# Optimization experiments

Hardware: AMD Instinct MI355X
Metric: run time of the kernel (lower is better)

Reference implementation:

```python
import jax, jax.numpy as jnp
import numpy as np
from jax import lax

DIM = 256
HEADS = 8
DIM_HEAD = 32
INNER = HEADS * DIM_HEAD  # 256
SCALE = DIM_HEAD ** -0.5
EPS = 1e-5
DN = ('NCHW', 'OIHW', 'NCHW')


def chan_layer_norm(x, g):
    # LayerNorm over channel dim (axis=1), biased variance
    mean = jnp.mean(x, axis=1, keepdims=True)
    var = jnp.mean((x - mean) ** 2, axis=1, keepdims=True)
    return (x - mean) / jnp.sqrt(var + EPS) * g


def conv1x1(x, w):
    return lax.conv_general_dilated(x, w, (1, 1), 'VALID', dimension_numbers=DN)


def dwconv3x3(x, w):
    # depthwise 3x3, padding=1, groups=channels; w: [C,1,3,3]
    return lax.conv_general_dilated(x, w, (1, 1), 'SAME', dimension_numbers=DN,
                                    feature_group_count=x.shape[1])


def setup_inputs() -> dict:
    key = jax.random.key(0)
    ks = jax.random.split(key, 9)
    B, X, Y = 16, 64, 64
    fmap = jax.random.normal(ks[0], (B, DIM, X, Y), dtype=jnp.float32)
    w = lambda k, shape: (jax.random.normal(k, shape, dtype=jnp.float32) * 0.02)
    return {
        'fmap': fmap,
        'g_norm': jnp.ones((1, DIM, 1, 1), dtype=jnp.float32),
        'wq1': w(ks[1], (INNER, DIM, 1, 1)),
        'wq_dw': w(ks[2], (INNER, 1, 3, 3)),
        'wk1': w(ks[3], (INNER, DIM, 1, 1)),
        'wk_dw': w(ks[4], (INNER, 1, 3, 3)),
        'wv1': w(ks[5], (INNER, DIM, 1, 1)),
        'wv_dw': w(ks[6], (INNER, 1, 3, 3)),
        'wo': w(ks[7], (DIM, INNER, 1, 1)),
        'g_out': jnp.ones((1, DIM, 1, 1), dtype=jnp.float32),
    }


def reference(fmap, g_norm, wq1, wq_dw, wk1, wk_dw, wv1, wv_dw, wo, g_out):
    b, _, X, Y = fmap.shape
    n = X * Y
    x = chan_layer_norm(fmap, g_norm)
    # QKV: 1x1 conv -> depthwise 3x3 conv (dropout is identity in eval)
    q = dwconv3x3(conv1x1(x, wq1), wq_dw)
    k = dwconv3x3(conv1x1(x, wk1), wk_dw)
    v = dwconv3x3(conv1x1(x, wv1), wv_dw)
    # b (h c) x y -> b h n c
    def split(t):
        return t.reshape(b, HEADS, DIM_HEAD, n).transpose(0, 1, 3, 2)
    q, k, v = split(q), split(k), split(v)
    q = jax.nn.softmax(q, axis=-1) * SCALE   # softmax over feature dim
    k = jax.nn.softmax(k, axis=-2)           # softmax over sequence dim
    ctx = jnp.einsum('bhnd,bhne->bhde', k, v)    # [b,h,d,d]
    out = jnp.einsum('bhnd,bhde->bhne', q, ctx)  # [b,h,n,d]
    # b h n d -> b (h d) x y
    out = out.transpose(0, 1, 3, 2).reshape(b, INNER, X, Y)
    out = jax.nn.silu(out)
    out = conv1x1(out, wo)
    return chan_layer_norm(out, g_out)
```

## Files before the change

kernel.cpp:

```cpp
#include <hip/hip_runtime.h>


typedef unsigned short u16;
typedef __bf16 bf16x8 __attribute__((ext_vector_type(8)));
typedef float f32x4 __attribute__((ext_vector_type(4)));
typedef float f32x16 __attribute__((ext_vector_type(16)));

#define DEV static __device__ __forceinline__

DEV float b2f(u16 u) { return __uint_as_float(((unsigned int)u) << 16); }
DEV u16 f2bf(float f) {
  unsigned int u = __float_as_uint(f);
  return (u16)((u + 0x7fffu + ((u >> 16) & 1u)) >> 16);
}
DEV void gl2lds16(const void* g, void* l) {
  __builtin_amdgcn_global_load_lds((__attribute__((address_space(1))) void*)g,
                                   (__attribute__((address_space(3))) void*)l, 16, 0, 0);
}

__global__ __launch_bounds__(256) void prep_kernel(const float* __restrict__ wk,
                                                   const float* __restrict__ wv,
                                                   const float* __restrict__ wq,
                                                   const float* __restrict__ wo,
                                                   u16* __restrict__ wb) {
  const int i = blockIdx.x * 256 + threadIdx.x;
  const int yb = blockIdx.y;
  if (yb == 0)      wb[(i >> 8) * 512 + (i & 255)] = f2bf(wk[i]);
  else if (yb == 1) wb[(i >> 8) * 512 + 256 + (i & 255)] = f2bf(wv[i]);
  else if (yb == 2) wb[131072 + i] = f2bf(wq[i]);
  else              wb[196608 + i] = f2bf(wo[i]);
}

__global__ __launch_bounds__(256) void ln_tin_kernel(const float* __restrict__ f,
                                                     const float* __restrict__ g,
                                                     u16* __restrict__ xT) {
  __shared__ u16 tile[64 * 268];
  __shared__ float red[2 * 256];
  __shared__ float mu_s[64], inv_s[64];
  const int t = threadIdx.x;
  const int p0 = blockIdx.x * 64;
  const int b = blockIdx.y;
  const long fb = (long)b * 256 * 4096;
  const int p = t & 63, cg = t >> 6;
  float s1 = 0.f, s2 = 0.f;
  for (int pass = 0; pass < 64; ++pass) {
    int c = pass * 4 + cg;
    float v = f[fb + (long)c * 4096 + p0 + p];
    s1 += v; s2 += v * v;
    tile[p * 268 + c] = f2bf(v);
  }
  red[cg * 64 + p] = s1;
  red[256 + cg * 64 + p] = s2;
  __syncthreads();
  if (t < 64) {
    float a1 = red[t] + red[64 + t] + red[128 + t] + red[192 + t];
    float a2 = red[256 + t] + red[320 + t] + red[384 + t] + red[448 + t];
    float mu = a1 * (1.f / 256.f);
    float var = a2 * (1.f / 256.f) - mu * mu;
    mu_s[t] = mu;
    inv_s[t] = 1.0f / sqrtf(var + 1e-5f);
  }
  __syncthreads();
  {
    const int ch8 = (t & 31) * 8, wp = t >> 5;
    float ga[8];
#pragma unroll
    for (int e = 0; e < 8; ++e) ga[e] = g[ch8 + e];
#pragma unroll
    for (int pass = 0; pass < 8; ++pass) {
      const int px = pass * 8 + wp;
      uint2 lo = *(const uint2*)&tile[px * 268 + ch8];
      uint2 hi = *(const uint2*)&tile[px * 268 + ch8 + 4];
      const u16* sl = (const u16*)&lo;
      const u16* sh = (const u16*)&hi;
      const float mu = mu_s[px], inv = inv_s[px];
      uint4 o;
      u16* os = (u16*)&o;
#pragma unroll
      for (int e = 0; e < 4; ++e) os[e] = f2bf((b2f(sl[e]) - mu) * inv * ga[e]);
#pragma unroll
      for (int e = 0; e < 4; ++e) os[4 + e] = f2bf((b2f(sh[e]) - mu) * inv * ga[4 + e]);
      *(uint4*)&xT[((long)b * 4096 + p0 + px) * 256 + ch8] = o;
    }
  }
}

__global__ __launch_bounds__(256) void gemm_bt_kernel(
    const u16* __restrict__ A, const u16* __restrict__ B0, const u16* __restrict__ B1,
    u16* __restrict__ Cg, int ldc, long sA, long sC) {
  __shared__ u16 As[128 * 32];
  __shared__ u16 Bs[128 * 32];
  const int t = threadIdx.x;
  const int wave = t >> 6, lane = t & 63, quad = lane >> 4, l16 = lane & 15;
  const int wr = wave >> 1, wc = wave & 1;
  const int m0 = blockIdx.x * 128;
  const int jt = blockIdx.y;
  const int b = blockIdx.z;
  const u16* Ab = A + (long)b * sA + (long)m0 * 256;
  const u16* Bt = (jt < 2 ? B0 : B1) + (jt & 1) * 128 * 256;
  u16* Cb = Cg + (long)b * sC + (long)m0 * ldc + jt * 128;

  const int srow = lane >> 2;
  const int scol = (lane & 3) * 8;
  f32x4 acc[4][4];
#pragma unroll
  for (int i = 0; i < 4; ++i)
#pragma unroll
    for (int j = 0; j < 4; ++j) acc[i][j] = (f32x4){0.f, 0.f, 0.f, 0.f};

  const int aoff = (wr * 64 + l16) * 32 + quad * 8;
  const int boff = (wc * 64 + l16) * 32 + quad * 8;

  for (int ks = 0; ks < 8; ++ks) {
    const int k0 = ks * 32;
    __syncthreads();
    for (int i = wave; i < 8; i += 4) {
      gl2lds16(Ab + (i * 16 + srow) * 256 + k0 + scol, &As[i * 512 + lane * 8]);
      gl2lds16(Bt + (i * 16 + srow) * 256 + k0 + scol, &Bs[i * 512 + lane * 8]);
    }
    __syncthreads();
    bf16x8 af[4], bfr[4];
#pragma unroll
    for (int mt = 0; mt < 4; ++mt) af[mt] = *(const bf16x8*)&As[aoff + mt * 512];
#pragma unroll
    for (int nt = 0; nt < 4; ++nt) bfr[nt] = *(const bf16x8*)&Bs[boff + nt * 512];
#pragma unroll
    for (int mt = 0; mt < 4; ++mt)
#pragma unroll
      for (int nt = 0; nt < 4; ++nt)
        acc[mt][nt] = __builtin_amdgcn_mfma_f32_16x16x32_bf16(af[mt], bfr[nt], acc[mt][nt], 0, 0, 0);
  }
#pragma unroll
  for (int mt = 0; mt < 4; ++mt) {
    const int mbase = wr * 64 + mt * 16 + quad * 4;
#pragma unroll
    for (int nt = 0; nt < 4; ++nt) {
      const int n = wc * 64 + nt * 16 + l16;
#pragma unroll
      for (int r = 0; r < 4; ++r)
        Cb[(long)(mbase + r) * ldc + n] = f2bf(acc[mt][nt][r]);
    }
  }
}

__global__ __launch_bounds__(256) void dwq_kernel(const u16* __restrict__ qT,
                                                  const float* __restrict__ wdw,
                                                  u16* __restrict__ qp) {
  __shared__ u16 tile[6 * 66 * 40];
  const int t = threadIdx.x;
  const int strip = blockIdx.x, h = blockIdx.y, b = blockIdx.z;
  const int x0 = strip * 4;
  const int wave = t >> 6, lane = t & 63;
  const int ysel = lane & 15, cg = lane >> 4;
  const int y = wave * 16 + ysel;
  const int ty = t >> 2, tc = t & 3;

  if (t < 48) {
    const int slot = t >> 3, brd = (t >> 2) & 1, c4 = t & 3;
    *(uint4*)&tile[slot * 2640 + (brd ? 65 * 40 : 0) + c4 * 8] = (uint4){0, 0, 0, 0};
  }
  const u16* qrow = qT + (long)b * 4096 * 256 + h * 32 + tc * 8;
#pragma unroll
  for (int s = 0; s < 6; ++s) {
    const int xx = x0 - 1 + s;
    uint4 v = (uint4){0, 0, 0, 0};
    if ((unsigned)xx < 64u) v = *(const uint4*)(qrow + (long)(xx * 64 + ty) * 256);
    *(uint4*)&tile[s * 2640 + (ty + 1) * 40 + tc * 8] = v;
  }
  float w[72];
#pragma unroll
  for (int q = 0; q < 8; ++q)
#pragma unroll
    for (int i = 0; i < 9; ++i) w[q * 9 + i] = wdw[(h * 32 + cg * 8 + q) * 9 + i];
  __syncthreads();

  u16* ob = qp + ((long)b * 4096 + y) * 256 + h * 32 + cg * 8;
#pragma unroll
  for (int it = 0; it < 4; ++it) {
    const int x = x0 + it;
    float acc[8] = {0.f, 0.f, 0.f, 0.f, 0.f, 0.f, 0.f, 0.f};
#pragma unroll
    for (int r = 0; r < 3; ++r) {
#pragma unroll
      for (int dy = 0; dy < 3; ++dy) {
        uint4 pk = *(const uint4*)&tile[(it + r) * 2640 + (y + dy) * 40 + cg * 8];
        const u16* s = (const u16*)&pk;
#pragma unroll
        for (int q = 0; q < 8; ++q)
          acc[q] = fmaf(w[q * 9 + r * 3 + dy], b2f(s[q]), acc[q]);
      }
    }
    float e[8];
    float s = 0.f;
#pragma unroll
    for (int q = 0; q < 8; ++q) { e[q] = __expf(acc[q]); s += e[q]; }
    s += __shfl_xor(s, 16);
    s += __shfl_xor(s, 32);
    const float inv = 0.17677669529663687f / s;
    uint4 o;
    u16* os = (u16*)&o;
#pragma unroll
    for (int q = 0; q < 8; ++q) os[q] = f2bf(e[q] * inv);
    *(uint4*)(ob + (long)x * 16384) = o;
  }
}

__global__ __launch_bounds__(1024, 4) void ctx_kernel(const u16* __restrict__ kvT,
                                                      const float* __restrict__ wkdw,
                                                      const float* __restrict__ wvdw,
                                                      float* __restrict__ par0,
                                                      float* __restrict__ par1) {
  __shared__ float redb[8 * 1088];
  __shared__ float redk[16 * 32];
  const int t = threadIdx.x;
  const int strip = blockIdx.x, h = blockIdx.y, b = blockIdx.z;
  const int wave = t >> 6, lane = t & 63;
  const int g = wave >> 2, wq = wave & 3;
  const int x0 = strip * 32 + g * 8;
  const int c = lane & 31, half = lane >> 5;
  const int ystart = wq * 16 + half * 8;
  float wk[9], wv[9];
#pragma unroll
  for (int i = 0; i < 9; ++i) {
    wk[i] = wkdw[(h * 32 + c) * 9 + i];
    wv[i] = wvdw[(h * 32 + c) * 9 + i];
  }
  const u16* kb = kvT + (long)b * 4096 * 512 + 2 * (h * 32 + c);

  float fk[3][10], fv[3][10];
  unsigned pk[10];
#pragma unroll
  for (int r = 0; r < 2; ++r) {
    const int x = x0 - 1 + r;
#pragma unroll
    for (int m = 0; m < 10; ++m) {
      const int yy = ystart - 1 + m;
      float a = 0.f, bb = 0.f;
      if (((unsigned)x < 64u) & ((unsigned)yy < 64u)) {
        const unsigned u = *(const unsigned*)(kb + (long)(x * 64 + yy) * 512);
        a = b2f((u16)(u & 0xffffu));
        bb = b2f((u16)(u >> 16));
      }
      fk[r][m] = a; fv[r][m] = bb;
    }
  }
#pragma unroll
  for (int m = 0; m < 10; ++m) {
    const int yy = ystart - 1 + m;
    unsigned u = 0;
    if (((unsigned)(x0 + 1) < 64u) & ((unsigned)yy < 64u))
      u = *(const unsigned*)(kb + (long)((x0 + 1) * 64 + yy) * 512);
    pk[m] = u;
  }
#pragma unroll
  for (int m = 0; m < 10; ++m) {
    fk[2][m] = __uint_as_float(pk[m] << 16);
    fv[2][m] = __uint_as_float(pk[m] & 0xffff0000u);
  }
  f32x16 acc;
#pragma unroll
  for (int r = 0; r < 16; ++r) acc[r] = 0.f;
  float ks = 0.f;

  for (int it = 0; it < 8; ++it) {
    const int xn = x0 + it + 2;
#pragma unroll
    for (int m = 0; m < 10; ++m) {
      const int yy = ystart - 1 + m;
      unsigned u = 0;
      if (((unsigned)xn < 64u) & ((unsigned)yy < 64u))
        u = *(const unsigned*)(kb + (long)(xn * 64 + yy) * 512);
      pk[m] = u;
    }
    union { bf16x8 v; u16 s[8]; } af, bf_;
#pragma unroll
    for (int j = 0; j < 8; ++j) {
      float a = 0.f, bb = 0.f;
#pragma unroll
      for (int r = 0; r < 3; ++r)
#pragma unroll
        for (int dy = 0; dy < 3; ++dy) {
          a = fmaf(wk[r * 3 + dy], fk[r][j + dy], a);
          bb = fmaf(wv[r * 3 + dy], fv[r][j + dy], bb);
        }
      const u16 eb = f2bf(__expf(a));
      ks += b2f(eb);
      af.s[j] = eb;
      bf_.s[j] = f2bf(bb);
    }
    acc = __builtin_amdgcn_mfma_f32_32x32x16_bf16(af.v, bf_.v, acc, 0, 0, 0);
#pragma unroll
    for (int m = 0; m < 10; ++m) {
      fk[0][m] = fk[1][m]; fv[0][m] = fv[1][m];
      fk[1][m] = fk[2][m]; fv[1][m] = fv[2][m];
      fk[2][m] = __uint_as_float(pk[m] << 16);
      fv[2][m] = __uint_as_float(pk[m] & 0xffff0000u);
    }
  }
  ks += __shfl_xor(ks, 32);
  if (half == 0) redk[wave * 32 + c] = ks;
  if (wave >= 8) {
#pragma unroll
    for (int r = 0; r < 16; ++r) redb[(wave - 8) * 1088 + lane * 17 + r] = acc[r];
  }
  __syncthreads();
  if (wave < 8) {
#pragma unroll
    for (int r = 0; r < 16; ++r) acc[r] += redb[wave * 1088 + lane * 17 + r];
  }
  __syncthreads();
  if (wave >= 4 && wave < 8) {
#pragma unroll
    for (int r = 0; r < 16; ++r) redb[(wave - 4) * 1088 + lane * 17 + r] = acc[r];
  }
  __syncthreads();
  if (wave < 4) {
#pragma unroll
    for (int r = 0; r < 16; ++r) acc[r] += redb[wave * 1088 + lane * 17 + r];
  }
  __syncthreads();
  if (wave >= 1 && wave < 4) {
#pragma unroll
    for (int r = 0; r < 16; ++r) redb[(wave - 1) * 1088 + lane * 17 + r] = acc[r];
  }
  __syncthreads();
  if (wave == 0) {
    float* par = (strip ? par1 : par0) + (long)(b * 8 + h) * 1056;
#pragma unroll
    for (int r = 0; r < 16; ++r) {
      float sum = acc[r] + redb[lane * 17 + r] + redb[1088 + lane * 17 + r] +
                  redb[2176 + lane * 17 + r];
      const int d = (r & 3) + 8 * (r >> 2) + 4 * half;
      par[d * 32 + c] = sum;
    }
    if (t < 32) {
      float s = 0.f;
#pragma unroll
      for (int w = 0; w < 16; ++w) s += redk[w * 32 + t];
      par[1024 + t] = s;
    }
  }
}

__global__ __launch_bounds__(256) void attn_o_ln_kernel(const u16* __restrict__ qp,
                                                        const float* __restrict__ par0,
                                                        const float* __restrict__ par1,
                                                        const u16* __restrict__ wo_bf,
                                                        const float* __restrict__ gout,
                                                        float* __restrict__ out) {
  __shared__ char smem[77312];
  u16* cnhi = (u16*)smem;
  u16* cnlo = (u16*)(smem + 20480);
  u16* ytile = (u16*)smem;
  u16* stile = (u16*)(smem + 40960);
  float* redS = (float*)(smem + 74752);
  float* redQ = (float*)(smem + 75776);
  float* mu_s = (float*)(smem + 76800);
  float* inv_s = (float*)(smem + 77056);
  const int t = threadIdx.x;
  const int p0 = blockIdx.x * 64;
  const int b = blockIdx.z;
  const int wave = t >> 6, lane = t & 63, quad = lane >> 4, l16 = lane & 15;

  for (int j = 0; j < 32; ++j) {
    const int lidx = j * 256 + t;
    const int e = lidx & 31, d = (lidx >> 5) & 31, h = lidx >> 10;
    const long base = (long)(b * 8 + h) * 1056;
    const float ks = par0[base + 1024 + d] + par1[base + 1024 + d];
    const float c = (par0[base + d * 32 + e] + par1[base + d * 32 + e]) / ks;
    const u16 hi = f2bf(c);
    cnhi[h * 1280 + e * 40 + d] = hi;
    cnlo[h * 1280 + e * 40 + d] = f2bf(c - b2f(hi));
  }
  __syncthreads();

  {
    const u16* qb = qp + ((long)b * 4096 + p0 + wave * 16) * 256;
    const int srow = wave * 16 + quad * 4;
#pragma unroll
    for (int h = 0; h < 8; ++h) {
      const int cb = h * 1280 + quad * 8;
      const bf16x8 bhi0 = *(const bf16x8*)&cnhi[cb + l16 * 40];
      const bf16x8 bhi1 = *(const bf16x8*)&cnhi[cb + (16 + l16) * 40];
      const bf16x8 blo0 = *(const bf16x8*)&cnlo[cb + l16 * 40];
      const bf16x8 blo1 = *(const bf16x8*)&cnlo[cb + (16 + l16) * 40];
      const bf16x8 af = *(const bf16x8*)&qb[l16 * 256 + h * 32 + quad * 8];
      f32x4 a0 = (f32x4){0.f, 0.f, 0.f, 0.f};
      f32x4 a1 = (f32x4){0.f, 0.f, 0.f, 0.f};
      a0 = __builtin_amdgcn_mfma_f32_16x16x32_bf16(af, blo0, a0, 0, 0, 0);
      a0 = __builtin_amdgcn_mfma_f32_16x16x32_bf16(af, bhi0, a0, 0, 0, 0);
      a1 = __builtin_amdgcn_mfma_f32_16x16x32_bf16(af, blo1, a1, 0, 0, 0);
      a1 = __builtin_amdgcn_mfma_f32_16x16x32_bf16(af, bhi1, a1, 0, 0, 0);
#pragma unroll
      for (int r = 0; r < 4; ++r) {
        const int row = srow + r;
        const float v0 = a0[r], v1 = a1[r];
        stile[row * 264 + h * 32 + l16] = f2bf(v0 / (1.f + __expf(-v0)));
        stile[row * 264 + h * 32 + 16 + l16] = f2bf(v1 / (1.f + __expf(-v1)));
      }
    }
  }
  __syncthreads();

  {
    const int n0 = wave * 64;
    f32x4 acc[4][4];
#pragma unroll
    for (int i = 0; i < 4; ++i)
#pragma unroll
      for (int j = 0; j < 4; ++j) acc[i][j] = (f32x4){0.f, 0.f, 0.f, 0.f};
#pragma unroll
    for (int ks = 0; ks < 8; ++ks) {
      const int k0 = ks * 32;
      bf16x8 af[4], bfr[4];
#pragma unroll
      for (int mt = 0; mt < 4; ++mt)
        af[mt] = *(const bf16x8*)&stile[(mt * 16 + l16) * 264 + k0 + quad * 8];
#pragma unroll
      for (int nt = 0; nt < 4; ++nt)
        bfr[nt] = *(const bf16x8*)&wo_bf[(n0 + nt * 16 + l16) * 256 + k0 + quad * 8];
#pragma unroll
      for (int mt = 0; mt < 4; ++mt)
#pragma unroll
        for (int nt = 0; nt < 4; ++nt)
          acc[mt][nt] = __builtin_amdgcn_mfma_f32_16x16x32_bf16(af[mt], bfr[nt], acc[mt][nt], 0, 0, 0);
    }
#pragma unroll
    for (int mt = 0; mt < 4; ++mt) {
      const int rb = mt * 16 + quad * 4;
      float ls1[4] = {0.f, 0.f, 0.f, 0.f};
      float ls2[4] = {0.f, 0.f, 0.f, 0.f};
#pragma unroll
      for (int nt = 0; nt < 4; ++nt) {
        const int col = n0 + nt * 16 + l16;
#pragma unroll
        for (int r = 0; r < 4; ++r) {
          const u16 bv = f2bf(acc[mt][nt][r]);
          ytile[(rb + r) * 258 + col] = bv;
          const float yb = b2f(bv);
          ls1[r] += yb;
          ls2[r] += yb * yb;
        }
      }
#pragma unroll
      for (int r = 0; r < 4; ++r) {
        float a = ls1[r], q2 = ls2[r];
        a += __shfl_xor(a, 1); q2 += __shfl_xor(q2, 1);
        a += __shfl_xor(a, 2); q2 += __shfl_xor(q2, 2);
        a += __shfl_xor(a, 4); q2 += __shfl_xor(q2, 4);
        a += __shfl_xor(a, 8); q2 += __shfl_xor(q2, 8);
        if (l16 == 0) {
          redS[(rb + r) * 4 + wave] = a;
          redQ[(rb + r) * 4 + wave] = q2;
        }
      }
    }
  }
  __syncthreads();

  if (t < 64) {
    float s1 = redS[t * 4] + redS[t * 4 + 1] + redS[t * 4 + 2] + redS[t * 4 + 3];
    float s2 = redQ[t * 4] + redQ[t * 4 + 1] + redQ[t * 4 + 2] + redQ[t * 4 + 3];
    float mu = s1 * (1.f / 256.f);
    float var = s2 * (1.f / 256.f) - mu * mu;
    mu_s[t] = mu;
    inv_s[t] = 1.0f / sqrtf(var + 1e-5f);
  }
  __syncthreads();
  {
    const int lpx = t & 63, cw = t >> 6;
    const long ob = (long)b * 256 * 4096;
    const float mu = mu_s[lpx], inv = inv_s[lpx];
#pragma unroll
    for (int pass = 0; pass < 16; ++pass) {
      const int c4 = pass * 16 + cw * 4;
      const unsigned w0 = *(const unsigned*)&ytile[lpx * 258 + c4];
      const unsigned w1 = *(const unsigned*)&ytile[lpx * 258 + c4 + 2];
      out[ob + (long)(c4 + 0) * 4096 + p0 + lpx] = (b2f((u16)(w0 & 0xffffu)) - mu) * inv * gout[c4 + 0];
      out[ob + (long)(c4 + 1) * 4096 + p0 + lpx] = (b2f((u16)(w0 >> 16)) - mu) * inv * gout[c4 + 1];
      out[ob + (long)(c4 + 2) * 4096 + p0 + lpx] = (b2f((u16)(w1 & 0xffffu)) - mu) * inv * gout[c4 + 2];
      out[ob + (long)(c4 + 3) * 4096 + p0 + lpx] = (b2f((u16)(w1 >> 16)) - mu) * inv * gout[c4 + 3];
    }
  }
}

extern "C" void kernel_launch(void* const* d_in, const int* in_sizes, int n_in,
                              void* d_out, int out_size, void* d_ws, size_t ws_size,
                              hipStream_t stream) {
  (void)in_sizes; (void)n_in; (void)out_size; (void)ws_size;
  const float* fmap = (const float*)d_in[0];
  const float* gnorm = (const float*)d_in[1];
  const float* wq1 = (const float*)d_in[2];
  const float* wqdw = (const float*)d_in[3];
  const float* wk1 = (const float*)d_in[4];
  const float* wkdw = (const float*)d_in[5];
  const float* wv1 = (const float*)d_in[6];
  const float* wvdw = (const float*)d_in[7];
  const float* wo = (const float*)d_in[8];
  const float* gout = (const float*)d_in[9];
  float* out = (float*)d_out;
  char* ws = (char*)d_ws;

  float* par0 = (float*)(ws);
  u16* wb = (u16*)(ws + 540672);
  float* par1 = (float*)(ws + 1064960);
  u16* wkv_bf = wb;
  u16* wq_bf = wb + 131072;
  u16* wo_bf = wb + 196608;
  u16* xT = (u16*)(ws + 2097152);
  u16* kvT = (u16*)(ws + 35651584);
  u16* qT = kvT;
  u16* qp = (u16*)(ws + 69206016);

  prep_kernel<<<dim3(256, 4), 256, 0, stream>>>(wk1, wv1, wq1, wo, wb);
  ln_tin_kernel<<<dim3(64, 16), 256, 0, stream>>>(fmap, gnorm, xT);
  gemm_bt_kernel<<<dim3(32, 4, 16), 256, 0, stream>>>(xT, wkv_bf, wkv_bf + 65536, kvT, 512,
                                                      4096L * 256, 4096L * 512);
  ctx_kernel<<<dim3(2, 8, 16), 1024, 0, stream>>>(kvT, wkdw, wvdw, par0, par1);
  gemm_bt_kernel<<<dim3(32, 2, 16), 256, 0, stream>>>(xT, wq_bf, wq_bf, qT, 256,
                                                      4096L * 256, 4096L * 256);
  dwq_kernel<<<dim3(16, 8, 16), 256, 0, stream>>>(qT, wqdw, qp);
  attn_o_ln_kernel<<<dim3(64, 1, 16), 256, 0, stream>>>(qp, par0, par1, wo_bf, gout, out);
}
```

Measured before the change: 311.1 us.

## Double attn_o_ln block to 512 threads with transposed MFMA and packed LDS stores

The final attention/output-projection/LayerNorm kernel now runs 8 waves per block instead of 4. The q·ctx stage splits heads across wave pairs, and the output GEMM gives each wave 32 output channels instead of 64. Operand order in both MFMA stages is swapped so results land contiguously per lane, which allows packed 32/64-bit LDS stores and a cheaper cross-quad row reduction. The aim is more latency hiding and fewer scalar LDS writes, at the cost of slightly more LDS, more reduction partials per row and one less block resident per CU.

```diff
diff --git a/kernel.cpp b/kernel.cpp
--- a/kernel.cpp
+++ b/kernel.cpp
@@ -342,125 +342,131 @@
   }
 }
 
-__global__ __launch_bounds__(256) void attn_o_ln_kernel(const u16* __restrict__ qp,
+__global__ __launch_bounds__(512) void attn_o_ln_kernel(const u16* __restrict__ qp,
                                                         const float* __restrict__ par0,
                                                         const float* __restrict__ par1,
                                                         const u16* __restrict__ wo_bf,
                                                         const float* __restrict__ gout,
                                                         float* __restrict__ out) {
-  __shared__ char smem[77312];
+  __shared__ char smem[79872];
   u16* cnhi = (u16*)smem;
   u16* cnlo = (u16*)(smem + 20480);
   u16* ytile = (u16*)smem;
   u16* stile = (u16*)(smem + 40960);
   float* redS = (float*)(smem + 74752);
-  float* redQ = (float*)(smem + 75776);
-  float* mu_s = (float*)(smem + 76800);
-  float* inv_s = (float*)(smem + 77056);
+  float* redQ = (float*)(smem + 77056);
+  float* mu_s = (float*)(smem + 79360);
+  float* inv_s = (float*)(smem + 79616);
   const int t = threadIdx.x;
   const int p0 = blockIdx.x * 64;
   const int b = blockIdx.z;
   const int wave = t >> 6, lane = t & 63, quad = lane >> 4, l16 = lane & 15;
 
-  for (int j = 0; j < 32; ++j) {
-    const int lidx = j * 256 + t;
-    const int e = lidx & 31, d = (lidx >> 5) & 31, h = lidx >> 10;
+#pragma unroll
+  for (int j = 0; j < 8; ++j) {
+    const int idx2 = j * 512 + t;
+    const int d0 = (idx2 & 15) * 2, e = (idx2 >> 4) & 31, h = idx2 >> 9;
     const long base = (long)(b * 8 + h) * 1056;
-    const float ks = par0[base + 1024 + d] + par1[base + 1024 + d];
-    const float c = (par0[base + d * 32 + e] + par1[base + d * 32 + e]) / ks;
-    const u16 hi = f2bf(c);
-    cnhi[h * 1280 + e * 40 + d] = hi;
-    cnlo[h * 1280 + e * 40 + d] = f2bf(c - b2f(hi));
+    const float ks0 = par0[base + 1024 + d0] + par1[base + 1024 + d0];
+    const float ks1 = par0[base + 1025 + d0] + par1[base + 1025 + d0];
+    const float c0 = (par0[base + d0 * 32 + e] + par1[base + d0 * 32 + e]) / ks0;
+    const float c1 = (par0[base + (d0 + 1) * 32 + e] + par1[base + (d0 + 1) * 32 + e]) / ks1;
+    const u16 h0 = f2bf(c0), h1 = f2bf(c1);
+    const u16 l0 = f2bf(c0 - b2f(h0)), l1 = f2bf(c1 - b2f(h1));
+    const int addr = h * 1280 + e * 40 + d0;
+    *(unsigned*)&cnhi[addr] = (unsigned)h0 | ((unsigned)h1 << 16);
+    *(unsigned*)&cnlo[addr] = (unsigned)l0 | ((unsigned)l1 << 16);
   }
   __syncthreads();
 
   {
-    const u16* qb = qp + ((long)b * 4096 + p0 + wave * 16) * 256;
-    const int srow = wave * 16 + quad * 4;
-#pragma unroll
-    for (int h = 0; h < 8; ++h) {
+    const int rg = wave & 3;
+    const int hb = (wave >> 2) * 4;
+    const u16* qb = qp + ((long)b * 4096 + p0 + rg * 16) * 256;
+#pragma unroll
+    for (int hi = 0; hi < 4; ++hi) {
+      const int h = hb + hi;
       const int cb = h * 1280 + quad * 8;
-      const bf16x8 bhi0 = *(const bf16x8*)&cnhi[cb + l16 * 40];
-      const bf16x8 bhi1 = *(const bf16x8*)&cnhi[cb + (16 + l16) * 40];
-      const bf16x8 blo0 = *(const bf16x8*)&cnlo[cb + l16 * 40];
-      const bf16x8 blo1 = *(const bf16x8*)&cnlo[cb + (16 + l16) * 40];
-      const bf16x8 af = *(const bf16x8*)&qb[l16 * 256 + h * 32 + quad * 8];
+      const bf16x8 chi0 = *(const bf16x8*)&cnhi[cb + l16 * 40];
+      const bf16x8 chi1 = *(const bf16x8*)&cnhi[cb + (16 + l16) * 40];
+      const bf16x8 clo0 = *(const bf16x8*)&cnlo[cb + l16 * 40];
+      const bf16x8 clo1 = *(const bf16x8*)&cnlo[cb + (16 + l16) * 40];
+      const bf16x8 qf = *(const bf16x8*)&qb[l16 * 256 + h * 32 + quad * 8];
       f32x4 a0 = (f32x4){0.f, 0.f, 0.f, 0.f};
       f32x4 a1 = (f32x4){0.f, 0.f, 0.f, 0.f};
-      a0 = __builtin_amdgcn_mfma_f32_16x16x32_bf16(af, blo0, a0, 0, 0, 0);
-      a0 = __builtin_amdgcn_mfma_f32_16x16x32_bf16(af, bhi0, a0, 0, 0, 0);
-      a1 = __builtin_amdgcn_mfma_f32_16x16x32_bf16(af, blo1, a1, 0, 0, 0);
-      a1 = __builtin_amdgcn_mfma_f32_16x16x32_bf16(af, bhi1, a1, 0, 0, 0);
+      a0 = __builtin_amdgcn_mfma_f32_16x16x32_bf16(clo0, qf, a0, 0, 0, 0);
+      a0 = __builtin_amdgcn_mfma_f32_16x16x32_bf16(chi0, qf, a0, 0, 0, 0);
+      a1 = __builtin_amdgcn_mfma_f32_16x16x32_bf16(clo1, qf, a1, 0, 0, 0);
+      a1 = __builtin_amdgcn_mfma_f32_16x16x32_bf16(chi1, qf, a1, 0, 0, 0);
+      const int sbase = (rg * 16 + l16) * 264 + h * 32 + quad * 4;
+      u16 v[8];
 #pragma unroll
       for (int r = 0; r < 4; ++r) {
-        const int row = srow + r;
-        const float v0 = a0[r], v1 = a1[r];
-        stile[row * 264 + h * 32 + l16] = f2bf(v0 / (1.f + __expf(-v0)));
-        stile[row * 264 + h * 32 + 16 + l16] = f2bf(v1 / (1.f + __expf(-v1)));
+        const float x0v = a0[r], x1v = a1[r];
+        v[r] = f2bf(x0v / (1.f + __expf(-x0v)));
+        v[4 + r] = f2bf(x1v / (1.f + __expf(-x1v)));
       }
+      *(uint2*)&stile[sbase] =
+          (uint2){(unsigned)v[0] | ((unsigned)v[1] << 16), (unsigned)v[2] | ((unsigned)v[3] << 16)};
+      *(uint2*)&stile[sbase + 16] =
+          (uint2){(unsigned)v[4] | ((unsigned)v[5] << 16), (unsigned)v[6] | ((unsigned)v[7] << 16)};
     }
   }
   __syncthreads();
 
   {
-    const int n0 = wave * 64;
-    f32x4 acc[4][4];
+    const int n0 = wave * 32;
+    f32x4 acc[4][2];
 #pragma unroll
     for (int i = 0; i < 4; ++i)
 #pragma unroll
-      for (int j = 0; j < 4; ++j) acc[i][j] = (f32x4){0.f, 0.f, 0.f, 0.f};
+      for (int j = 0; j < 2; ++j) acc[i][j] = (f32x4){0.f, 0.f, 0.f, 0.f};
 #pragma unroll
     for (int ks = 0; ks < 8; ++ks) {
       const int k0 = ks * 32;
-      bf16x8 af[4], bfr[4];
-#pragma unroll
-      for (int mt = 0; mt < 4; ++mt)
-        af[mt] = *(const bf16x8*)&stile[(mt * 16 + l16) * 264 + k0 + quad * 8];
-#pragma unroll
-      for (int nt = 0; nt < 4; ++nt)
-        bfr[nt] = *(const bf16x8*)&wo_bf[(n0 + nt * 16 + l16) * 256 + k0 + quad * 8];
-#pragma unroll
-      for (int mt = 0; mt < 4; ++mt)
-#pragma unroll
-        for (int nt = 0; nt < 4; ++nt)
-          acc[mt][nt] = __builtin_amdgcn_mfma_f32_16x16x32_bf16(af[mt], bfr[nt], acc[mt][nt], 0, 0, 0);
-    }
-#pragma unroll
-    for (int mt = 0; mt < 4; ++mt) {
-      const int rb = mt * 16 + quad * 4;
-      float ls1[4] = {0.f, 0.f, 0.f, 0.f};
-      float ls2[4] = {0.f, 0.f, 0.f, 0.f};
-#pragma unroll
-      for (int nt = 0; nt < 4; ++nt) {
-        const int col = n0 + nt * 16 + l16;
+      bf16x8 sf[4], wf[2];
+#pragma unroll
+      for (int pt = 0; pt < 4; ++pt)
+        sf[pt] = *(const bf16x8*)&stile[(pt * 16 + l16) * 264 + k0 + quad * 8];
+#pragma unroll
+      for (int nt = 0; nt < 2; ++nt)
+        wf[nt] = *(const bf16x8*)&wo_bf[(n0 + nt * 16 + l16) * 256 + k0 + quad * 8];
+#pragma unroll
+      for (int pt = 0; pt < 4; ++pt)
+#pragma unroll
+        for (int nt = 0; nt < 2; ++nt)
+          acc[pt][nt] = __builtin_amdgcn_mfma_f32_16x16x32_bf16(wf[nt], sf[pt], acc[pt][nt], 0, 0, 0);
+    }
+#pragma unroll
+    for (int pt = 0; pt < 4; ++pt) {
+      float ls1 = 0.f, ls2 = 0.f;
+#pragma unroll
+      for (int nt = 0; nt < 2; ++nt) {
+        u16 bv[4];
 #pragma unroll
         for (int r = 0; r < 4; ++r) {
-          const u16 bv = f2bf(acc[mt][nt][r]);
-          ytile[(rb + r) * 258 + col] = bv;
-          const float yb = b2f(bv);
-          ls1[r] += yb;
-          ls2[r] += yb * yb;
+          bv[r] = f2bf(acc[pt][nt][r]);
+          const float yb = b2f(bv[r]);
+          ls1 += yb; ls2 += yb * yb;
         }
+        const int ybase = (pt * 16 + l16) * 274 + n0 + nt * 16 + quad * 4;
+        *(unsigned*)&ytile[ybase] = (unsigned)bv[0] | ((unsigned)bv[1] << 16);
+        *(unsigned*)&ytile[ybase + 2] = (unsigned)bv[2] | ((unsigned)bv[3] << 16);
       }
-#pragma unroll
-      for (int r = 0; r < 4; ++r) {
-        float a = ls1[r], q2 = ls2[r];
-        a += __shfl_xor(a, 1); q2 += __shfl_xor(q2, 1);
-        a += __shfl_xor(a, 2); q2 += __shfl_xor(q2, 2);
-        a += __shfl_xor(a, 4); q2 += __shfl_xor(q2, 4);
-        a += __shfl_xor(a, 8); q2 += __shfl_xor(q2, 8);
-        if (l16 == 0) {
-          redS[(rb + r) * 4 + wave] = a;
-          redQ[(rb + r) * 4 + wave] = q2;
-        }
+      ls1 += __shfl_xor(ls1, 16); ls2 += __shfl_xor(ls2, 16);
+      ls1 += __shfl_xor(ls1, 32); ls2 += __shfl_xor(ls2, 32);
+      if (quad == 0) {
+        redS[(pt * 16 + l16) * 9 + wave] = ls1;
+        redQ[(pt * 16 + l16) * 9 + wave] = ls2;
       }
     }
   }
   __syncthreads();
 
   if (t < 64) {
-    float s1 = redS[t * 4] + redS[t * 4 + 1] + redS[t * 4 + 2] + redS[t * 4 + 3];
-    float s2 = redQ[t * 4] + redQ[t * 4 + 1] + redQ[t * 4 + 2] + redQ[t * 4 + 3];
+    float s1 = 0.f, s2 = 0.f;
+#pragma unroll
+    for (int w = 0; w < 8; ++w) { s1 += redS[t * 9 + w]; s2 += redQ[t * 9 + w]; }
     float mu = s1 * (1.f / 256.f);
     float var = s2 * (1.f / 256.f) - mu * mu;
     mu_s[t] = mu;
@@ -472,10 +478,10 @@
     const long ob = (long)b * 256 * 4096;
     const float mu = mu_s[lpx], inv = inv_s[lpx];
 #pragma unroll
-    for (int pass = 0; pass < 16; ++pass) {
-      const int c4 = pass * 16 + cw * 4;
-      const unsigned w0 = *(const unsigned*)&ytile[lpx * 258 + c4];
-      const unsigned w1 = *(const unsigned*)&ytile[lpx * 258 + c4 + 2];
+    for (int pass = 0; pass < 8; ++pass) {
+      const int c4 = pass * 32 + cw * 4;
+      const unsigned w0 = *(const unsigned*)&ytile[lpx * 274 + c4];
+      const unsigned w1 = *(const unsigned*)&ytile[lpx * 274 + c4 + 2];
       out[ob + (long)(c4 + 0) * 4096 + p0 + lpx] = (b2f((u16)(w0 & 0xffffu)) - mu) * inv * gout[c4 + 0];
       out[ob + (long)(c4 + 1) * 4096 + p0 + lpx] = (b2f((u16)(w0 >> 16)) - mu) * inv * gout[c4 + 1];
       out[ob + (long)(c4 + 2) * 4096 + p0 + lpx] = (b2f((u16)(w1 & 0xffffu)) - mu) * inv * gout[c4 + 2];
@@ -520,5 +526,5 @@
   gemm_bt_kernel<<<dim3(32, 2, 16), 256, 0, stream>>>(xT, wq_bf, wq_bf, qT, 256,
                                                       4096L * 256, 4096L * 256);
   dwq_kernel<<<dim3(16, 8, 16), 256, 0, stream>>>(qT, wqdw, qp);
-  attn_o_ln_kernel<<<dim3(64, 1, 16), 256, 0, stream>>>(qp, par0, par1, wo_bf, gout, out);
-}
+  attn_o_ln_kernel<<<dim3(64, 1, 16), 512, 0, stream>>>(qp, par0, par1, wo_bf, gout, out);
+}
```

After: 312.4 us. No clear change (+0.4%).
